# Kernel optimization log

Hardware: AMD Instinct MI355X
Metric: run time of the kernel (lower is better)

The kernel has to match this reference:

```python
import jax, jax.numpy as jnp
import numpy as np


def _apply_rope(t, cos, sin):
    # t: [b, s, h, d]; cos/sin: [s, d//2]; interleaved complex rotation
    b, s, h, d = t.shape
    tr = t.reshape(b, s, h, d // 2, 2)
    a, bb = tr[..., 0], tr[..., 1]
    c = cos[None, :, None, :]
    si = sin[None, :, None, :]
    out_r = a * c - bb * si
    out_i = a * si + bb * c
    return jnp.stack([out_r, out_i], axis=-1).reshape(b, s, h, d)


def setup_inputs() -> dict:
    key = jax.random.key(0)
    ks = jax.random.split(key, 10)
    B, S, D = 4, 512, 4096
    H, HKV, HD = 32, 8, 128
    START = 512
    wscale = 0.02  # keep activations in sane range
    x = jax.random.normal(ks[0], (B, S, D), dtype=jnp.float32)
    wq = jax.random.normal(ks[1], (H * HD, D), dtype=jnp.float32) * wscale
    wk = jax.random.normal(ks[2], (HKV * HD, D), dtype=jnp.float32) * wscale
    wv = jax.random.normal(ks[3], (HKV * HD, D), dtype=jnp.float32) * wscale
    wo = jax.random.normal(ks[4], (D, H * HD), dtype=jnp.float32) * wscale
    # RoPE angles for absolute positions [START, START+S)
    theta = 500000.0
    inv_freq = 1.0 / (theta ** (np.arange(0, HD, 2, dtype=np.float32) / HD))
    pos = np.arange(START, START + S, dtype=np.float32)
    ang = pos[:, None] * inv_freq[None, :]  # [S, HD//2]
    freqs_cos = jnp.asarray(np.cos(ang), dtype=jnp.float32)
    freqs_sin = jnp.asarray(np.sin(ang), dtype=jnp.float32)
    cache_k = jax.random.normal(ks[5], (B, START, HKV, HD), dtype=jnp.float32)
    cache_v = jax.random.normal(ks[6], (B, START, HKV, HD), dtype=jnp.float32)
    return {"x": x, "wq": wq, "wk": wk, "wv": wv, "wo": wo,
            "freqs_cos": freqs_cos, "freqs_sin": freqs_sin,
            "cache_k": cache_k, "cache_v": cache_v, "start_pos": START}


def reference(x, wq, wk, wv, wo, freqs_cos, freqs_sin, cache_k, cache_v, start_pos):
    B, S, D = x.shape
    H = wq.shape[0] // 128
    HKV = wk.shape[0] // 128
    HD = 128
    n_rep = H // HKV
    # QKV projections (Linear: y = x @ W^T)
    xq = jnp.einsum('bsd,ed->bse', x, wq).reshape(B, S, H, HD)
    xk = jnp.einsum('bsd,ed->bse', x, wk).reshape(B, S, HKV, HD)
    xv = jnp.einsum('bsd,ed->bse', x, wv).reshape(B, S, HKV, HD)
    # rotary embedding on new q/k
    xq = _apply_rope(xq, freqs_cos, freqs_sin)
    xk = _apply_rope(xk, freqs_cos, freqs_sin)
    # append new k/v to cache -> total kv length T = start_pos + S
    keys = jnp.concatenate([cache_k, xk], axis=1)    # [B, T, HKV, HD]
    values = jnp.concatenate([cache_v, xv], axis=1)  # [B, T, HKV, HD]
    # GQA: repeat kv heads (repeat_interleave along head dim)
    keys = jnp.repeat(keys, n_rep, axis=2)      # [B, T, H, HD]
    values = jnp.repeat(values, n_rep, axis=2)  # [B, T, H, HD]
    scores = jnp.einsum('bqhd,bkhd->bhqk', xq, keys) / jnp.sqrt(jnp.float32(HD))
    # causal mask: query abs pos start_pos+i attends to kv pos <= start_pos+i
    T = start_pos + S
    q_pos = start_pos + jnp.arange(S)
    k_pos = jnp.arange(T)
    mask = k_pos[None, :] <= q_pos[:, None]  # [S, T]
    scores = jnp.where(mask[None, None, :, :], scores, -jnp.inf)
    probs = jax.nn.softmax(scores.astype(jnp.float32), axis=-1).astype(x.dtype)
    out = jnp.einsum('bhqk,bkhd->bqhd', probs, values).reshape(B, S, H * HD)
    return jnp.einsum('bse,de->bsd', out, wo)
```

## Files before the change

kernel.cpp:

```cpp
#include <hip/hip_runtime.h>
#include <hip/hip_bf16.h>


#define B_ 4
#define S_ 512
#define D_ 4096
#define H_ 32
#define HKV_ 8
#define HD_ 128
#define T_ 1024
#define M_ 2048
#define NQKV_ 6144

typedef __attribute__((ext_vector_type(8))) short bf16x8;
typedef __attribute__((ext_vector_type(4))) float f32x4;

#define GLOAD_LDS16(g, l)                                                     \
  __builtin_amdgcn_global_load_lds(                                           \
      (const __attribute__((address_space(1))) void*)(g),                     \
      (__attribute__((address_space(3))) void*)(l), 16, 0, 0)

__global__ void cvt_f32_bf16(const float* __restrict__ in,
                             __hip_bfloat16* __restrict__ out, long n) {
  long i = ((long)blockIdx.x * blockDim.x + threadIdx.x) * 4;
  if (i >= n) return;
  float4 v = *(const float4*)(in + i);
  __hip_bfloat16 t[4] = {__float2bfloat16(v.x), __float2bfloat16(v.y),
                         __float2bfloat16(v.z), __float2bfloat16(v.w)};
  *(uint2*)(out + i) = *(const uint2*)t;
}

__global__ __launch_bounds__(512, 2) void gemm256(
    const __hip_bfloat16* __restrict__ A, const __hip_bfloat16* __restrict__ B,
    float* __restrict__ C, int M, int N, int K, long ldA, long ldB, long ldC) {
  const int nbx = N >> 8;
  const int nwg = nbx * (M >> 8);
  const int lin = blockIdx.x + nbx * blockIdx.y;
  const int cpx = nwg >> 3;
  const int swz = (lin & 7) * cpx + (lin >> 3);
  const int m0 = (swz / nbx) << 8;
  const int n0 = (swz - (swz / nbx) * nbx) << 8;

  const int tid = threadIdx.x;
  const int w = tid >> 6, l = tid & 63;
  const int wm = w >> 2, wn = w & 3;
  const int lr = l & 15, lq = l >> 4;

  __shared__ __align__(16) __hip_bfloat16 smem[8][8192];

  const int rS = w * 16 + (l >> 2);
  const int cS = (l & 3) ^ ((rS >> 1) & 3);
  const __hip_bfloat16* gA = A + (long)(m0 + rS) * ldA + cS * 8;
  const __hip_bfloat16* gB = B + (long)(n0 + rS) * ldB + cS * 8;
  const long stA = 128 * ldA, stB = 128 * ldB;
  const int wofs = w * 512;

  const int cR = (lq ^ ((lr >> 1) & 3)) * 8;
  const int aOff = (wm * 128 + lr) * 32 + cR;
  const int bOff = (wn * 64 + lr) * 32 + cR;

  f32x4 acc[8][4];
#pragma unroll
  for (int i = 0; i < 8; i++)
#pragma unroll
    for (int j = 0; j < 4; j++) acc[i][j] = f32x4{0.f, 0.f, 0.f, 0.f};

  const int nkt = K >> 6;

#define STAGE_A(buf, kh, ko)                                  \
  {                                                           \
    const __hip_bfloat16* g_ = gA + (ko) + (kh) * 32;         \
    __hip_bfloat16* d_ = &smem[(buf) * 4 + (kh)][wofs];       \
    GLOAD_LDS16(g_, d_);                                      \
    GLOAD_LDS16(g_ + stA, d_ + 4096);                         \
  }
#define STAGE_B(buf, kh, ko)                                  \
  {                                                           \
    const __hip_bfloat16* g_ = gB + (ko) + (kh) * 32;         \
    __hip_bfloat16* d_ = &smem[(buf) * 4 + 2 + (kh)][wofs];   \
    GLOAD_LDS16(g_, d_);                                      \
    GLOAD_LDS16(g_ + stB, d_ + 4096);                         \
  }

  STAGE_A(0, 0, 0);
  STAGE_B(0, 0, 0);
  STAGE_A(0, 1, 0);
  STAGE_B(0, 1, 0);
  asm volatile("s_waitcnt vmcnt(4)" ::: "memory");
  __builtin_amdgcn_s_barrier();

  bf16x8 af[4], bfr[4];
  for (int t = 0; t < nkt; ++t) {
    const int b = t & 1;
    int tn = t + 1;
    if (tn == nkt) tn = 0;
    const long ko = (long)tn << 6;
    const __hip_bfloat16* rA0 = &smem[b * 4 + 0][0];
    const __hip_bfloat16* rA1 = &smem[b * 4 + 1][0];
    const __hip_bfloat16* rB0 = &smem[b * 4 + 2][0];
    const __hip_bfloat16* rB1 = &smem[b * 4 + 3][0];

#pragma unroll
    for (int i = 0; i < 4; i++) af[i] = *(const bf16x8*)(rA0 + aOff + i * 512);
#pragma unroll
    for (int j = 0; j < 4; j++) bfr[j] = *(const bf16x8*)(rB0 + bOff + j * 512);
    STAGE_A(b ^ 1, 0, ko);
    __builtin_amdgcn_s_barrier();
    __builtin_amdgcn_s_setprio(1);
#pragma unroll
    for (int i = 0; i < 4; i++)
#pragma unroll
      for (int j = 0; j < 4; j++)
        acc[i][j] = __builtin_amdgcn_mfma_f32_16x16x32_bf16(af[i], bfr[j],
                                                            acc[i][j], 0, 0, 0);
    __builtin_amdgcn_s_setprio(0);
    __builtin_amdgcn_s_barrier();

#pragma unroll
    for (int i = 0; i < 4; i++)
      af[i] = *(const bf16x8*)(rA0 + aOff + (i + 4) * 512);
    STAGE_B(b ^ 1, 0, ko);
    asm volatile("s_waitcnt vmcnt(4)" ::: "memory");
    __builtin_amdgcn_s_barrier();
    __builtin_amdgcn_s_setprio(1);
#pragma unroll
    for (int i = 0; i < 4; i++)
#pragma unroll
      for (int j = 0; j < 4; j++)
        acc[i + 4][j] = __builtin_amdgcn_mfma_f32_16x16x32_bf16(
            af[i], bfr[j], acc[i + 4][j], 0, 0, 0);
    __builtin_amdgcn_s_setprio(0);
    __builtin_amdgcn_s_barrier();

#pragma unroll
    for (int i = 0; i < 4; i++) af[i] = *(const bf16x8*)(rA1 + aOff + i * 512);
#pragma unroll
    for (int j = 0; j < 4; j++) bfr[j] = *(const bf16x8*)(rB1 + bOff + j * 512);
    STAGE_A(b ^ 1, 1, ko);
    __builtin_amdgcn_s_barrier();
    __builtin_amdgcn_s_setprio(1);
#pragma unroll
    for (int i = 0; i < 4; i++)
#pragma unroll
      for (int j = 0; j < 4; j++)
        acc[i][j] = __builtin_amdgcn_mfma_f32_16x16x32_bf16(af[i], bfr[j],
                                                            acc[i][j], 0, 0, 0);
    __builtin_amdgcn_s_setprio(0);
    __builtin_amdgcn_s_barrier();

#pragma unroll
    for (int i = 0; i < 4; i++)
      af[i] = *(const bf16x8*)(rA1 + aOff + (i + 4) * 512);
    STAGE_B(b ^ 1, 1, ko);
    asm volatile("s_waitcnt vmcnt(4)" ::: "memory");
    __builtin_amdgcn_s_barrier();
    __builtin_amdgcn_s_setprio(1);
#pragma unroll
    for (int i = 0; i < 4; i++)
#pragma unroll
      for (int j = 0; j < 4; j++)
        acc[i + 4][j] = __builtin_amdgcn_mfma_f32_16x16x32_bf16(
            af[i], bfr[j], acc[i + 4][j], 0, 0, 0);
    __builtin_amdgcn_s_setprio(0);
    __builtin_amdgcn_s_barrier();
  }
  asm volatile("s_waitcnt vmcnt(0)" ::: "memory");

#undef STAGE_A
#undef STAGE_B

  const int crow = m0 + wm * 128 + lq * 4;
  const int ccol = n0 + wn * 64 + lr;
#pragma unroll
  for (int i = 0; i < 8; i++)
#pragma unroll
    for (int j = 0; j < 4; j++)
#pragma unroll
      for (int r = 0; r < 4; r++)
        C[(long)(crow + i * 16 + r) * ldC + (ccol + j * 16)] = acc[i][j][r];
}

__global__ __launch_bounds__(512, 2) void gemm128(
    const __hip_bfloat16* __restrict__ A, const __hip_bfloat16* __restrict__ B,
    float* __restrict__ C, int M, int N, int K, long ldA, long ldB, long ldC) {
  const int nbx = N >> 8;
  const int nwg = nbx * (M >> 7);
  const int lin = blockIdx.x + nbx * blockIdx.y;
  const int cpx = nwg >> 3;
  const int swz = (lin & 7) * cpx + (lin >> 3);
  const int by = swz / nbx;
  const int m0 = by << 7;
  const int n0 = (swz - by * nbx) << 8;

  const int tid = threadIdx.x;
  const int w = tid >> 6, l = tid & 63;
  const int wm = w >> 2, wn = w & 3;
  const int lr = l & 15, lq = l >> 4;

  __shared__ __align__(16) __hip_bfloat16 smem[3][24576];

  const int rS = w * 16 + (l >> 2);
  const int cS = (l & 3) ^ ((rS >> 1) & 3);
  const __hip_bfloat16* gA = A + (long)(m0 + rS) * ldA + cS * 8;
  const __hip_bfloat16* gB = B + (long)(n0 + rS) * ldB + cS * 8;
  const long stB = 128 * ldB;
  const int wofs = w * 512;

  const int cR = (lq ^ ((lr >> 1) & 3)) * 8;
  const int aOff = (wm * 64 + lr) * 32 + cR;
  const int bOff = (wn * 64 + lr) * 32 + cR;

  f32x4 acc[4][4];
#pragma unroll
  for (int i = 0; i < 4; i++)
#pragma unroll
    for (int j = 0; j < 4; j++) acc[i][j] = f32x4{0.f, 0.f, 0.f, 0.f};

  const int nkt = K >> 6;

#define STAGEF(buf, ko)                                            \
  {                                                                \
    const __hip_bfloat16* ga_ = gA + (ko);                         \
    GLOAD_LDS16(ga_, &smem[buf][wofs]);                            \
    GLOAD_LDS16(ga_ + 32, &smem[buf][4096 + wofs]);                \
    const __hip_bfloat16* gb_ = gB + (ko);                         \
    GLOAD_LDS16(gb_, &smem[buf][8192 + wofs]);                     \
    GLOAD_LDS16(gb_ + stB, &smem[buf][12288 + wofs]);              \
    GLOAD_LDS16(gb_ + 32, &smem[buf][16384 + wofs]);               \
    GLOAD_LDS16(gb_ + stB + 32, &smem[buf][20480 + wofs]);         \
  }

  STAGEF(0, 0);
  STAGEF(1, 64);
  asm volatile("s_waitcnt vmcnt(6)" ::: "memory");
  __builtin_amdgcn_s_barrier();

  int bc = 0, b1 = 1, b2 = 2;
  bf16x8 af[4], bfr[4];
  for (int t = 0; t < nkt; ++t) {
    int t2 = t + 2;
    if (t2 >= nkt) t2 -= nkt;
    const long ko2 = (long)t2 << 6;
    STAGEF(b2, ko2);

    const __hip_bfloat16* rA = &smem[bc][0];
    const __hip_bfloat16* rB = &smem[bc][8192];

#pragma unroll
    for (int i = 0; i < 4; i++) af[i] = *(const bf16x8*)(rA + aOff + i * 512);
#pragma unroll
    for (int j = 0; j < 4; j++) bfr[j] = *(const bf16x8*)(rB + bOff + j * 512);
    __builtin_amdgcn_s_setprio(1);
#pragma unroll
    for (int i = 0; i < 4; i++)
#pragma unroll
      for (int j = 0; j < 4; j++)
        acc[i][j] = __builtin_amdgcn_mfma_f32_16x16x32_bf16(af[i], bfr[j],
                                                            acc[i][j], 0, 0, 0);
    __builtin_amdgcn_s_setprio(0);

#pragma unroll
    for (int i = 0; i < 4; i++)
      af[i] = *(const bf16x8*)(rA + 4096 + aOff + i * 512);
#pragma unroll
    for (int j = 0; j < 4; j++)
      bfr[j] = *(const bf16x8*)(rB + 8192 + bOff + j * 512);
    __builtin_amdgcn_s_setprio(1);
#pragma unroll
    for (int i = 0; i < 4; i++)
#pragma unroll
      for (int j = 0; j < 4; j++)
        acc[i][j] = __builtin_amdgcn_mfma_f32_16x16x32_bf16(af[i], bfr[j],
                                                            acc[i][j], 0, 0, 0);
    __builtin_amdgcn_s_setprio(0);

    asm volatile("s_waitcnt lgkmcnt(0)" ::: "memory");
    __builtin_amdgcn_sched_barrier(0);
    asm volatile("s_waitcnt vmcnt(6)" ::: "memory");
    __builtin_amdgcn_s_barrier();

    int tmp = bc; bc = b1; b1 = b2; b2 = tmp;
  }
  asm volatile("s_waitcnt vmcnt(0)" ::: "memory");

#undef STAGEF

  const int crow = m0 + wm * 64 + lq * 4;
  const int ccol = n0 + wn * 64 + lr;
#pragma unroll
  for (int i = 0; i < 4; i++)
#pragma unroll
    for (int j = 0; j < 4; j++)
#pragma unroll
      for (int r = 0; r < 4; r++)
        C[(long)(crow + i * 16 + r) * ldC + (ccol + j * 16)] = acc[i][j][r];
}

__global__ __launch_bounds__(256, 2) void flash_attn(
    const __hip_bfloat16* __restrict__ qb,
    const __hip_bfloat16* __restrict__ kb,
    const __hip_bfloat16* __restrict__ vtb,
    __hip_bfloat16* __restrict__ ob) {
  const int qt = 3 - blockIdx.x;
  const int z = blockIdx.y;
  const int b = z >> 5, h = z & 31, kvh = h >> 2;
  const int q0 = qt * 128;
  const int tid = threadIdx.x, wave = tid >> 6, lane = tid & 63;
  const int lr = lane & 15, lq = lane >> 4;
  const int wrow = wave * 32;
  const float scale = 0.08838834764831845f;

  __shared__ __align__(16) __hip_bfloat16 smem[64 * 128 + 128 * 64 + 128 * 72];
  __hip_bfloat16* Ks = smem;
  __hip_bfloat16* Vs = smem + 64 * 128;
  __hip_bfloat16* Ps = smem + 64 * 128 + 128 * 64;
  __hip_bfloat16* Os = smem;

  const __hip_bfloat16* Kz = kb + ((long)(b * 8 + kvh)) * T_ * HD_;
  const __hip_bfloat16* Vz = vtb + ((long)(b * 8 + kvh)) * HD_ * T_;
  const __hip_bfloat16* Qz = qb + ((long)(b * 512 + q0)) * 4096 + h * 128;
  __hip_bfloat16* obz = ob + ((long)(b * 512 + q0)) * 4096 + h * 128;

  bf16x8 qf[2][4];
#pragma unroll
  for (int i = 0; i < 2; i++)
#pragma unroll
    for (int kb4 = 0; kb4 < 4; kb4++)
      qf[i][kb4] = *(const bf16x8*)(Qz + (long)(wrow + i * 16 + lr) * 4096 +
                                    kb4 * 32 + lq * 8);

  int kOff[4], vOff[4];
#pragma unroll
  for (int it = 0; it < 4; it++) {
    int G = it * 256 + tid;
    int t = G >> 4, ck = (G & 15) ^ (t & 7);
    kOff[it] = t * 128 + ck * 8;
    int d = G >> 3, cv = (G & 7) ^ (d & 7);
    vOff[it] = d * 1024 + cv * 8;
  }

  f32x4 O[2][8];
#pragma unroll
  for (int i = 0; i < 2; i++)
#pragma unroll
    for (int j = 0; j < 8; j++) O[i][j] = f32x4{0.f, 0.f, 0.f, 0.f};
  float mst[2][4], lst[2][4];
#pragma unroll
  for (int i = 0; i < 2; i++)
#pragma unroll
    for (int r = 0; r < 4; r++) {
      mst[i][r] = -1e30f;
      lst[i][r] = 0.f;
    }

  const int ntiles = 10 + 2 * qt, fulltiles = 8 + 2 * qt;
  const int hxor = lr & 7;

  for (int kt = 0; kt < ntiles; kt++) {
    const int k0 = kt * 64;
#pragma unroll
    for (int it = 0; it < 4; it++)
      GLOAD_LDS16(Kz + (long)k0 * 128 + kOff[it],
                  Ks + (it * 256 + wave * 64) * 8);
#pragma unroll
    for (int it = 0; it < 4; it++)
      GLOAD_LDS16(Vz + k0 + vOff[it], Vs + (it * 256 + wave * 64) * 8);
    __syncthreads();

    f32x4 s[2][4];
#pragma unroll
    for (int i = 0; i < 2; i++)
#pragma unroll
      for (int j = 0; j < 4; j++) s[i][j] = f32x4{0.f, 0.f, 0.f, 0.f};
#pragma unroll
    for (int kb4 = 0; kb4 < 4; kb4++) {
      bf16x8 kf[4];
#pragma unroll
      for (int j = 0; j < 4; j++)
        kf[j] = *(const bf16x8*)(Ks + (j * 16 + lr) * 128 +
                                 ((kb4 * 4 + lq) ^ hxor) * 8);
#pragma unroll
      for (int i = 0; i < 2; i++)
#pragma unroll
        for (int j = 0; j < 4; j++)
          s[i][j] = __builtin_amdgcn_mfma_f32_16x16x32_bf16(qf[i][kb4], kf[j],
                                                            s[i][j], 0, 0, 0);
    }

    const bool mt = (kt >= fulltiles);
#pragma unroll
    for (int i = 0; i < 2; i++)
#pragma unroll
      for (int j = 0; j < 4; j++)
#pragma unroll
        for (int r = 0; r < 4; r++) {
          float sv = s[i][j][r] * scale;
          if (mt) {
            int key = k0 + j * 16 + lr;
            int qp = 512 + q0 + wrow + i * 16 + lq * 4 + r;
            if (key > qp) sv = -1e30f;
          }
          s[i][j][r] = sv;
        }

    float al[2][4];
#pragma unroll
    for (int i = 0; i < 2; i++)
#pragma unroll
      for (int r = 0; r < 4; r++) {
        float mx = fmaxf(fmaxf(s[i][0][r], s[i][1][r]),
                         fmaxf(s[i][2][r], s[i][3][r]));
        mx = fmaxf(mx, __shfl_xor(mx, 1));
        mx = fmaxf(mx, __shfl_xor(mx, 2));
        mx = fmaxf(mx, __shfl_xor(mx, 4));
        mx = fmaxf(mx, __shfl_xor(mx, 8));
        float mn = fmaxf(mst[i][r], mx);
        al[i][r] = __expf(mst[i][r] - mn);
        mst[i][r] = mn;
      }
#pragma unroll
    for (int i = 0; i < 2; i++)
#pragma unroll
      for (int j = 0; j < 4; j++)
#pragma unroll
        for (int r = 0; r < 4; r++)
          s[i][j][r] = __expf(s[i][j][r] - mst[i][r]);
#pragma unroll
    for (int i = 0; i < 2; i++)
#pragma unroll
      for (int r = 0; r < 4; r++) {
        float sm = s[i][0][r] + s[i][1][r] + s[i][2][r] + s[i][3][r];
        sm += __shfl_xor(sm, 1);
        sm += __shfl_xor(sm, 2);
        sm += __shfl_xor(sm, 4);
        sm += __shfl_xor(sm, 8);
        lst[i][r] = lst[i][r] * al[i][r] + sm;
      }
#pragma unroll
    for (int i = 0; i < 2; i++)
#pragma unroll
      for (int j = 0; j < 8; j++)
#pragma unroll
        for (int r = 0; r < 4; r++) O[i][j][r] *= al[i][r];

#pragma unroll
    for (int i = 0; i < 2; i++)
#pragma unroll
      for (int j = 0; j < 4; j++)
#pragma unroll
        for (int r = 0; r < 4; r++)
          Ps[(wrow + i * 16 + lq * 4 + r) * 72 + j * 16 + lr] =
              __float2bfloat16(s[i][j][r]);

#pragma unroll
    for (int kc = 0; kc < 2; kc++) {
      bf16x8 pa[2];
#pragma unroll
      for (int i = 0; i < 2; i++)
        pa[i] = *(const bf16x8*)(Ps + (wrow + i * 16 + lr) * 72 + kc * 32 +
                                 lq * 8);
      bf16x8 vf[8];
#pragma unroll
      for (int j = 0; j < 8; j++)
        vf[j] = *(const bf16x8*)(Vs + (j * 16 + lr) * 64 +
                                 ((kc * 4 + lq) ^ hxor) * 8);
#pragma unroll
      for (int i = 0; i < 2; i++)
#pragma unroll
        for (int j = 0; j < 8; j++)
          O[i][j] = __builtin_amdgcn_mfma_f32_16x16x32_bf16(pa[i], vf[j],
                                                            O[i][j], 0, 0, 0);
    }
    __syncthreads();
  }

#pragma unroll
  for (int i = 0; i < 2; i++)
#pragma unroll
    for (int r = 0; r < 4; r++) {
      float inv = 1.f / lst[i][r];
#pragma unroll
      for (int j = 0; j < 8; j++)
        Os[(wrow + i * 16 + lq * 4 + r) * 136 + j * 16 + lr] =
            __float2bfloat16(O[i][j][r] * inv);
    }
  __syncthreads();
#pragma unroll
  for (int it = 0; it < 8; it++) {
    int G = it * 256 + tid;
    int m = G >> 4, c = G & 15;
    *(bf16x8*)(obz + (long)m * 4096 + c * 8) =
        *(const bf16x8*)(Os + m * 136 + c * 8);
  }
}

__global__ void rope_kernel(const float* __restrict__ qkv,
                            const float* __restrict__ fcos,
                            const float* __restrict__ fsin,
                            __hip_bfloat16* __restrict__ qb,
                            __hip_bfloat16* __restrict__ kb) {
  int m = blockIdx.y;
  int j = blockIdx.x * blockDim.x + threadIdx.x;
  if (j >= 2560) return;
  int s = m & (S_ - 1);
  long rowbase = (long)m * NQKV_;
  if (j < 2048) {
    int dpair = j & 63;
    float a = qkv[rowbase + 2 * j], bb = qkv[rowbase + 2 * j + 1];
    float c = fcos[s * 64 + dpair], si = fsin[s * 64 + dpair];
    long o = (long)m * 4096 + 2 * j;
    qb[o] = __float2bfloat16(a * c - bb * si);
    qb[o + 1] = __float2bfloat16(a * si + bb * c);
  } else {
    int j2 = j - 2048;
    int kvh = j2 >> 6, dpair = j2 & 63;
    float a = qkv[rowbase + 4096 + 2 * j2], bb = qkv[rowbase + 4096 + 2 * j2 + 1];
    float c = fcos[s * 64 + dpair], si = fsin[s * 64 + dpair];
    int b = m >> 9;
    long o = (((long)(b * HKV_ + kvh)) * T_ + 512 + s) * HD_ + 2 * dpair;
    kb[o] = __float2bfloat16(a * c - bb * si);
    kb[o + 1] = __float2bfloat16(a * si + bb * c);
  }
}

__global__ void kcache_cvt(const float* __restrict__ cache_k,
                           __hip_bfloat16* __restrict__ kb) {
  long i = (long)blockIdx.x * 256 + threadIdx.x;
  if (i >= (long)B_ * HKV_ * 512 * HD_) return;
  int d = i & 127;
  int t = (i >> 7) & 511;
  int kvh = (i >> 16) & 7;
  int b = i >> 19;
  long o = (((long)(b * HKV_ + kvh)) * T_ + t) * HD_ + d;
  kb[o] = __float2bfloat16(
      cache_k[(((long)(b * 512 + t)) * HKV_ + kvh) * HD_ + d]);
}

__global__ void v_transpose(const float* __restrict__ cache_v,
                            const float* __restrict__ qkv,
                            __hip_bfloat16* __restrict__ vtb) {
  __shared__ float tile[32][33];
  int t0 = blockIdx.x * 32, d0 = blockIdx.y * 32;
  int bk = blockIdx.z;
  int b = bk >> 3, kvh = bk & 7;
#pragma unroll
  for (int it = 0; it < 4; it++) {
    int t = t0 + threadIdx.y + it * 8;
    int d = d0 + threadIdx.x;
    float v;
    if (t < 512)
      v = cache_v[(((long)(b * 512 + t)) * HKV_ + kvh) * HD_ + d];
    else
      v = qkv[((long)(b * S_) + (t - 512)) * NQKV_ + 5120 + kvh * HD_ + d];
    tile[threadIdx.y + it * 8][threadIdx.x] = v;
  }
  __syncthreads();
#pragma unroll
  for (int it = 0; it < 4; it++) {
    int d = d0 + threadIdx.y + it * 8;
    int t = t0 + threadIdx.x;
    vtb[((long)bk * HD_ + d) * T_ + t] =
        __float2bfloat16(tile[threadIdx.x][threadIdx.y + it * 8]);
  }
}

extern "C" void kernel_launch(void* const* d_in, const int* in_sizes, int n_in,
                              void* d_out, int out_size, void* d_ws,
                              size_t ws_size, hipStream_t stream) {
  const float* x = (const float*)d_in[0];
  const float* wq = (const float*)d_in[1];
  const float* wk = (const float*)d_in[2];
  const float* wv = (const float*)d_in[3];
  const float* wo = (const float*)d_in[4];
  const float* fcos = (const float*)d_in[5];
  const float* fsin = (const float*)d_in[6];
  const float* cache_k = (const float*)d_in[7];
  const float* cache_v = (const float*)d_in[8];
  float* out = (float*)d_out;

  char* ws = (char*)d_ws;
  const size_t szR0 = (size_t)M_ * 4096 * 2;
  const size_t szR1 = (size_t)NQKV_ * D_ * 2;
  const size_t szR2 = (size_t)M_ * NQKV_ * 4;
  const size_t szKV = (size_t)B_ * HKV_ * T_ * HD_ * 2;

  size_t R0 = 0;
  size_t R1 = R0 + szR0;
  size_t R2 = R1 + szR1;
  size_t R3 = R2 + szR2;
  size_t R4 = R3 + szKV;

  __hip_bfloat16* xb = (__hip_bfloat16*)(ws + R0);
  __hip_bfloat16* wqkvb = (__hip_bfloat16*)(ws + R1);
  float* qkvf = (float*)(ws + R2);
  __hip_bfloat16* kb = (__hip_bfloat16*)(ws + R3);
  __hip_bfloat16* vtb = (__hip_bfloat16*)(ws + R4);

  dim3 blk(256);

  cvt_f32_bf16<<<(M_ * (long)D_ / 4 + 255) / 256, blk, 0, stream>>>(
      x, xb, (long)M_ * D_);
  cvt_f32_bf16<<<((long)D_ * D_ / 4 + 255) / 256, blk, 0, stream>>>(
      wq, wqkvb, (long)D_ * D_);
  cvt_f32_bf16<<<((long)1024 * D_ / 4 + 255) / 256, blk, 0, stream>>>(
      wk, wqkvb + (long)4096 * D_, (long)1024 * D_);
  cvt_f32_bf16<<<((long)1024 * D_ / 4 + 255) / 256, blk, 0, stream>>>(
      wv, wqkvb + (long)5120 * D_, (long)1024 * D_);

  gemm256<<<dim3(NQKV_ / 256, M_ / 256), dim3(512), 0, stream>>>(
      xb, wqkvb, qkvf, M_, NQKV_, D_, D_, D_, NQKV_);

  __hip_bfloat16* qb = xb;
  rope_kernel<<<dim3(10, M_), blk, 0, stream>>>(qkvf, fcos, fsin, qb, kb);

  kcache_cvt<<<((long)B_ * HKV_ * 512 * HD_ + 255) / 256, blk, 0, stream>>>(
      cache_k, kb);
  v_transpose<<<dim3(T_ / 32, HD_ / 32, B_ * HKV_), dim3(32, 8), 0, stream>>>(
      cache_v, qkvf, vtb);

  __hip_bfloat16* wob = wqkvb;
  cvt_f32_bf16<<<((long)D_ * D_ / 4 + 255) / 256, blk, 0, stream>>>(
      wo, wob, (long)D_ * D_);

  __hip_bfloat16* ob = xb;
  flash_attn<<<dim3(4, B_ * H_), blk, 0, stream>>>(qb, kb, vtb, ob);

  gemm128<<<dim3(D_ / 256, M_ / 128), dim3(512), 0, stream>>>(
      ob, wob, out, M_, D_, D_, D_, D_, D_);
}
```

Baseline: 496.0 us.

## Retile QKV GEMM to 256x192 tiles and register-prefetch K/V in attention

```diff
diff --git a/kernel.cpp b/kernel.cpp
--- a/kernel.cpp
+++ b/kernel.cpp
@@ -30,87 +30,77 @@
   *(uint2*)(out + i) = *(const uint2*)t;
 }
 
-__global__ __launch_bounds__(512, 2) void gemm256(
+__global__ __launch_bounds__(512, 2) void gemm_qkv(
     const __hip_bfloat16* __restrict__ A, const __hip_bfloat16* __restrict__ B,
-    float* __restrict__ C, int M, int N, int K, long ldA, long ldB, long ldC) {
-  const int nbx = N >> 8;
-  const int nwg = nbx * (M >> 8);
-  const int lin = blockIdx.x + nbx * blockIdx.y;
-  const int cpx = nwg >> 3;
-  const int swz = (lin & 7) * cpx + (lin >> 3);
-  const int m0 = (swz / nbx) << 8;
-  const int n0 = (swz - (swz / nbx) * nbx) << 8;
+    float* __restrict__ C, int K, long ldA, long ldB, long ldC) {
+  const int lin = blockIdx.x + 32 * blockIdx.y;
+  const int swz = (lin & 7) * 32 + (lin >> 3);
+  const int m0 = (swz >> 5) << 8;
+  const int n0 = (swz & 31) * 192;
 
   const int tid = threadIdx.x;
   const int w = tid >> 6, l = tid & 63;
   const int wm = w >> 2, wn = w & 3;
   const int lr = l & 15, lq = l >> 4;
 
-  __shared__ __align__(16) __hip_bfloat16 smem[8][8192];
-
-  const int rS = w * 16 + (l >> 2);
-  const int cS = (l & 3) ^ ((rS >> 1) & 3);
+  __shared__ __align__(16) __hip_bfloat16 smem[2][28672];
+
+  const int rS = w * 8 + (l >> 3);
+  const int cS = (l & 7) ^ (l >> 3);
   const __hip_bfloat16* gA = A + (long)(m0 + rS) * ldA + cS * 8;
   const __hip_bfloat16* gB = B + (long)(n0 + rS) * ldB + cS * 8;
-  const long stA = 128 * ldA, stB = 128 * ldB;
   const int wofs = w * 512;
 
-  const int cR = (lq ^ ((lr >> 1) & 3)) * 8;
-  const int aOff = (wm * 128 + lr) * 32 + cR;
-  const int bOff = (wn * 64 + lr) * 32 + cR;
-
-  f32x4 acc[8][4];
+  const int sl0 = (lq ^ (lr & 7)) * 8;
+  const int sl1 = ((4 + lq) ^ (lr & 7)) * 8;
+  const int aRow = (wm * 128 + lr) * 64;
+  const int bRow = (wn * 48 + lr) * 64;
+
+  f32x4 acc[8][3];
 #pragma unroll
   for (int i = 0; i < 8; i++)
 #pragma unroll
-    for (int j = 0; j < 4; j++) acc[i][j] = f32x4{0.f, 0.f, 0.f, 0.f};
+    for (int j = 0; j < 3; j++) acc[i][j] = f32x4{0.f, 0.f, 0.f, 0.f};
 
   const int nkt = K >> 6;
 
-#define STAGE_A(buf, kh, ko)                                  \
-  {                                                           \
-    const __hip_bfloat16* g_ = gA + (ko) + (kh) * 32;         \
-    __hip_bfloat16* d_ = &smem[(buf) * 4 + (kh)][wofs];       \
-    GLOAD_LDS16(g_, d_);                                      \
-    GLOAD_LDS16(g_ + stA, d_ + 4096);                         \
-  }
-#define STAGE_B(buf, kh, ko)                                  \
-  {                                                           \
-    const __hip_bfloat16* g_ = gB + (ko) + (kh) * 32;         \
-    __hip_bfloat16* d_ = &smem[(buf) * 4 + 2 + (kh)][wofs];   \
-    GLOAD_LDS16(g_, d_);                                      \
-    GLOAD_LDS16(g_ + stB, d_ + 4096);                         \
-  }
-
-  STAGE_A(0, 0, 0);
-  STAGE_B(0, 0, 0);
-  STAGE_A(0, 1, 0);
-  STAGE_B(0, 1, 0);
-  asm volatile("s_waitcnt vmcnt(4)" ::: "memory");
+#define STAGEQ(buf, ko)                                              \
+  {                                                                  \
+    GLOAD_LDS16(gA + (ko), &smem[buf][wofs]);                        \
+    GLOAD_LDS16(gA + 64 * ldA + (ko), &smem[buf][4096 + wofs]);      \
+    GLOAD_LDS16(gA + 128 * ldA + (ko), &smem[buf][8192 + wofs]);     \
+    GLOAD_LDS16(gA + 192 * ldA + (ko), &smem[buf][12288 + wofs]);    \
+    GLOAD_LDS16(gB + (ko), &smem[buf][16384 + wofs]);                \
+    GLOAD_LDS16(gB + 64 * ldB + (ko), &smem[buf][20480 + wofs]);     \
+    GLOAD_LDS16(gB + 128 * ldB + (ko), &smem[buf][24576 + wofs]);    \
+  }
+
+  STAGEQ(0, 0);
+  asm volatile("s_waitcnt vmcnt(0)" ::: "memory");
   __builtin_amdgcn_s_barrier();
 
-  bf16x8 af[4], bfr[4];
+  bf16x8 af[4], bfr[3];
   for (int t = 0; t < nkt; ++t) {
-    const int b = t & 1;
+    const int bc = t & 1;
     int tn = t + 1;
     if (tn == nkt) tn = 0;
     const long ko = (long)tn << 6;
-    const __hip_bfloat16* rA0 = &smem[b * 4 + 0][0];
-    const __hip_bfloat16* rA1 = &smem[b * 4 + 1][0];
-    const __hip_bfloat16* rB0 = &smem[b * 4 + 2][0];
-    const __hip_bfloat16* rB1 = &smem[b * 4 + 3][0];
-
-#pragma unroll
-    for (int i = 0; i < 4; i++) af[i] = *(const bf16x8*)(rA0 + aOff + i * 512);
-#pragma unroll
-    for (int j = 0; j < 4; j++) bfr[j] = *(const bf16x8*)(rB0 + bOff + j * 512);
-    STAGE_A(b ^ 1, 0, ko);
+    const __hip_bfloat16* rA = &smem[bc][0];
+    const __hip_bfloat16* rB = &smem[bc][16384];
+
+#pragma unroll
+    for (int i = 0; i < 4; i++)
+      af[i] = *(const bf16x8*)(rA + aRow + i * 1024 + sl0);
+#pragma unroll
+    for (int j = 0; j < 3; j++)
+      bfr[j] = *(const bf16x8*)(rB + bRow + j * 1024 + sl0);
+    STAGEQ(bc ^ 1, ko);
     __builtin_amdgcn_s_barrier();
     __builtin_amdgcn_s_setprio(1);
 #pragma unroll
     for (int i = 0; i < 4; i++)
 #pragma unroll
-      for (int j = 0; j < 4; j++)
+      for (int j = 0; j < 3; j++)
         acc[i][j] = __builtin_amdgcn_mfma_f32_16x16x32_bf16(af[i], bfr[j],
                                                             acc[i][j], 0, 0, 0);
     __builtin_amdgcn_s_setprio(0);
@@ -118,31 +108,30 @@
 
 #pragma unroll
     for (int i = 0; i < 4; i++)
-      af[i] = *(const bf16x8*)(rA0 + aOff + (i + 4) * 512);
-    STAGE_B(b ^ 1, 0, ko);
-    asm volatile("s_waitcnt vmcnt(4)" ::: "memory");
+      af[i] = *(const bf16x8*)(rA + aRow + (i + 4) * 1024 + sl0);
     __builtin_amdgcn_s_barrier();
     __builtin_amdgcn_s_setprio(1);
 #pragma unroll
     for (int i = 0; i < 4; i++)
 #pragma unroll
-      for (int j = 0; j < 4; j++)
+      for (int j = 0; j < 3; j++)
         acc[i + 4][j] = __builtin_amdgcn_mfma_f32_16x16x32_bf16(
             af[i], bfr[j], acc[i + 4][j], 0, 0, 0);
     __builtin_amdgcn_s_setprio(0);
     __builtin_amdgcn_s_barrier();
 
 #pragma unroll
-    for (int i = 0; i < 4; i++) af[i] = *(const bf16x8*)(rA1 + aOff + i * 512);
-#pragma unroll
-    for (int j = 0; j < 4; j++) bfr[j] = *(const bf16x8*)(rB1 + bOff + j * 512);
-    STAGE_A(b ^ 1, 1, ko);
+    for (int i = 0; i < 4; i++)
+      af[i] = *(const bf16x8*)(rA + aRow + i * 1024 + sl1);
+#pragma unroll
+    for (int j = 0; j < 3; j++)
+      bfr[j] = *(const bf16x8*)(rB + bRow + j * 1024 + sl1);
     __builtin_amdgcn_s_barrier();
     __builtin_amdgcn_s_setprio(1);
 #pragma unroll
     for (int i = 0; i < 4; i++)
 #pragma unroll
-      for (int j = 0; j < 4; j++)
+      for (int j = 0; j < 3; j++)
         acc[i][j] = __builtin_amdgcn_mfma_f32_16x16x32_bf16(af[i], bfr[j],
                                                             acc[i][j], 0, 0, 0);
     __builtin_amdgcn_s_setprio(0);
@@ -150,31 +139,28 @@
 
 #pragma unroll
     for (int i = 0; i < 4; i++)
-      af[i] = *(const bf16x8*)(rA1 + aOff + (i + 4) * 512);
-    STAGE_B(b ^ 1, 1, ko);
-    asm volatile("s_waitcnt vmcnt(4)" ::: "memory");
+      af[i] = *(const bf16x8*)(rA + aRow + (i + 4) * 1024 + sl1);
     __builtin_amdgcn_s_barrier();
     __builtin_amdgcn_s_setprio(1);
 #pragma unroll
     for (int i = 0; i < 4; i++)
 #pragma unroll
-      for (int j = 0; j < 4; j++)
+      for (int j = 0; j < 3; j++)
         acc[i + 4][j] = __builtin_amdgcn_mfma_f32_16x16x32_bf16(
             af[i], bfr[j], acc[i + 4][j], 0, 0, 0);
     __builtin_amdgcn_s_setprio(0);
-    __builtin_amdgcn_s_barrier();
-  }
-  asm volatile("s_waitcnt vmcnt(0)" ::: "memory");
-
-#undef STAGE_A
-#undef STAGE_B
+    asm volatile("s_waitcnt vmcnt(0)" ::: "memory");
+    __builtin_amdgcn_s_barrier();
+  }
+
+#undef STAGEQ
 
   const int crow = m0 + wm * 128 + lq * 4;
-  const int ccol = n0 + wn * 64 + lr;
+  const int ccol = n0 + wn * 48 + lr;
 #pragma unroll
   for (int i = 0; i < 8; i++)
 #pragma unroll
-    for (int j = 0; j < 4; j++)
+    for (int j = 0; j < 3; j++)
 #pragma unroll
       for (int r = 0; r < 4; r++)
         C[(long)(crow + i * 16 + r) * ldC + (ccol + j * 16)] = acc[i][j][r];
@@ -356,16 +342,33 @@
   const int ntiles = 10 + 2 * qt, fulltiles = 8 + 2 * qt;
   const int hxor = lr & 7;
 
+  bf16x8 kreg[4], vreg[4];
+#pragma unroll
+  for (int it = 0; it < 4; it++)
+    kreg[it] = *(const bf16x8*)(Kz + kOff[it]);
+#pragma unroll
+  for (int it = 0; it < 4; it++)
+    vreg[it] = *(const bf16x8*)(Vz + vOff[it]);
+
   for (int kt = 0; kt < ntiles; kt++) {
     const int k0 = kt * 64;
 #pragma unroll
     for (int it = 0; it < 4; it++)
-      GLOAD_LDS16(Kz + (long)k0 * 128 + kOff[it],
-                  Ks + (it * 256 + wave * 64) * 8);
+      *(bf16x8*)(Ks + (it * 256 + tid) * 8) = kreg[it];
 #pragma unroll
     for (int it = 0; it < 4; it++)
-      GLOAD_LDS16(Vz + k0 + vOff[it], Vs + (it * 256 + wave * 64) * 8);
-    __syncthreads();
+      *(bf16x8*)(Vs + (it * 256 + tid) * 8) = vreg[it];
+    if (kt + 1 < ntiles) {
+      const long kn = (long)(kt + 1) * 64;
+#pragma unroll
+      for (int it = 0; it < 4; it++)
+        kreg[it] = *(const bf16x8*)(Kz + kn * 128 + kOff[it]);
+#pragma unroll
+      for (int it = 0; it < 4; it++)
+        vreg[it] = *(const bf16x8*)(Vz + kn + vOff[it]);
+    }
+    asm volatile("s_waitcnt lgkmcnt(0)" ::: "memory");
+    __builtin_amdgcn_s_barrier();
 
     f32x4 s[2][4];
 #pragma unroll
@@ -471,7 +474,8 @@
           O[i][j] = __builtin_amdgcn_mfma_f32_16x16x32_bf16(pa[i], vf[j],
                                                             O[i][j], 0, 0, 0);
     }
-    __syncthreads();
+    asm volatile("s_waitcnt lgkmcnt(0)" ::: "memory");
+    __builtin_amdgcn_s_barrier();
   }
 
 #pragma unroll
@@ -607,8 +611,8 @@
   cvt_f32_bf16<<<((long)1024 * D_ / 4 + 255) / 256, blk, 0, stream>>>(
       wv, wqkvb + (long)5120 * D_, (long)1024 * D_);
 
-  gemm256<<<dim3(NQKV_ / 256, M_ / 256), dim3(512), 0, stream>>>(
-      xb, wqkvb, qkvf, M_, NQKV_, D_, D_, D_, NQKV_);
+  gemm_qkv<<<dim3(32, 8), dim3(512), 0, stream>>>(
+      xb, wqkvb, qkvf, D_, D_, D_, NQKV_);
 
   __hip_bfloat16* qb = xb;
   rope_kernel<<<dim3(10, M_), blk, 0, stream>>>(qkvf, fcos, fsin, qb, kb);
```

New measurement: 500.0 us. About the same (+0.8%).
